# Optimization experiments

Measured on AMD Instinct MI355X. Metric: run time of the kernel, lower is better.

## Reference

```python
import jax, jax.numpy as jnp
import numpy as np

WINDOW_SIZE = 2
SOFTMAX_TEMP = 0.01
WIDTH = 320
EPS = 1e-12  # F.normalize default eps


def _l2norm(x, axis):
    n = jnp.sqrt(jnp.sum(x * x, axis=axis, keepdims=True))
    return x / jnp.maximum(n, EPS)


def setup_inputs() -> dict:
    key = jax.random.key(0)
    k1, k2, k3, k4 = jax.random.split(key, 4)
    BW, C, N, S = 4, 256, 1024, 1
    return {
        "keypoint_scores": jax.random.uniform(k1, (BW, S, N), dtype=jnp.float32),
        "keypoint_desc": jax.random.normal(k2, (BW, C, N), dtype=jnp.float32),
        "desc_dense": jax.random.normal(k3, (BW, C, WIDTH, WIDTH), dtype=jnp.float32),
        "keypoint_coords": jax.random.uniform(k4, (BW, N, 2), dtype=jnp.float32),
    }


def reference(keypoint_scores, keypoint_desc, desc_dense, keypoint_coords):
    BW, C, N = keypoint_desc.shape
    B = BW // WINDOW_SIZE
    P = B * (WINDOW_SIZE - 1)  # number of (src, tgt) pairs

    # dense source pixel coordinates (u=col, v=row), matching torch meshgrid 'ij'
    idx = jnp.arange(WIDTH * WIDTH)
    coords = jnp.stack([(idx % WIDTH).astype(jnp.float32),
                        (idx // WIDTH).astype(jnp.float32)], axis=1)  # (HW, 2)

    # pair indexing: for window i, targets are i*w+1 .. i*w+w-1, source is i*w
    tgt_ids = jnp.array([i * WINDOW_SIZE + j for i in range(B)
                         for j in range(1, WINDOW_SIZE)], dtype=jnp.int32)
    src_ids = (tgt_ids // WINDOW_SIZE) * WINDOW_SIZE

    # normalized dense source descriptors: (B, C, HW)
    src_dense = desc_dense[::WINDOW_SIZE].reshape(B, C, -1)
    src_un = _l2norm(src_dense, axis=1)
    src_sel = src_un[tgt_ids // WINDOW_SIZE]  # (P, C, HW)

    # normalized target keypoint descriptors: (P, C, N)
    tgt_n = _l2norm(keypoint_desc[tgt_ids], axis=1)

    # QK^T over descriptor channel: (P, N, HW)
    match_vals = jnp.einsum('pcn,pcm->pnm', tgt_n, src_sel)
    soft = jax.nn.softmax(match_vals / SOFTMAX_TEMP, axis=2)

    # soft-argmax coordinates: (P, N, 2)
    pseudo_coords = jnp.einsum('pnm,md->pnd', soft, coords)

    match_weights = keypoint_scores[tgt_ids]  # (P, S, N)
    return pseudo_coords, match_weights, tgt_ids, src_ids
```

## Files before the change

### kernel.cpp

```cpp
#include <hip/hip_runtime.h>
#include <stdint.h>

#define HW_      102400
#define C_       256
#define N_       1024
#define P_       2
#define TILES_   1600
#define CHUNKS_  32
#define ITERS_   50
#define NB_      4
#define K2_      144.269504088896340f
#define MOFF_    (-72.134752044448170f)

typedef __attribute__((ext_vector_type(8))) short bf16x8;
typedef __attribute__((ext_vector_type(4))) float f32x4;

#define WS_TGT_OFF  0
#define WS_PAR_OFF  (1u << 20)
#define WS_PN_OFF   (4u << 20)

#define SWR(r) (((r) ^ ((r) >> 3)) & 7)

__device__ __forceinline__ uint32_t packbf(float a, float b) {
  uint32_t r;
  asm("v_cvt_pk_bf16_f32 %0, %1, %2" : "=v"(r) : "v"(a), "v"(b));
  return r;
}
__device__ __forceinline__ float fexp2(float x) {
  return __builtin_amdgcn_exp2f(x);
}
__device__ __forceinline__ void dma16(const uint32_t* g, uint32_t* l) {
  __builtin_amdgcn_global_load_lds(
      (const __attribute__((address_space(1))) uint32_t*)g,
      (__attribute__((address_space(3))) uint32_t*)l, 16, 0, 0);
}

__global__ __launch_bounds__(256)
void k_pre(const float* __restrict__ dense, const float* __restrict__ kdesc,
           const float* __restrict__ kscores, uint32_t* __restrict__ PN,
           uint16_t* __restrict__ tgt, float* __restrict__ out) {
  __shared__ float part[16][64];
  __shared__ float sinv[64];
  __shared__ uint32_t T[8192];
  const int bid = blockIdx.x;
  if (bid < P_ * TILES_) {
    const int p = bid / TILES_, tile = bid % TILES_;
    const int t   = threadIdx.x;
    const int px4 = (t & 15) * 4;
    const int cg  = t >> 4;
    const float* src = dense + (size_t)(p * 2) * C_ * HW_ + (size_t)(cg * 16) * HW_
                     + tile * 64 + px4;
    float v[16][4];
    #pragma unroll
    for (int cc = 0; cc < 16; ++cc) {
      const float4 q = *(const float4*)(src + (size_t)cc * HW_);
      v[cc][0] = q.x; v[cc][1] = q.y; v[cc][2] = q.z; v[cc][3] = q.w;
    }
    float ps[4] = {0.f, 0.f, 0.f, 0.f};
    #pragma unroll
    for (int cc = 0; cc < 16; ++cc) {
      #pragma unroll
      for (int i = 0; i < 4; ++i) ps[i] = fmaf(v[cc][i], v[cc][i], ps[i]);
    }
    #pragma unroll
    for (int i = 0; i < 4; ++i) part[cg][px4 + i] = ps[i];
    __syncthreads();
    if (t < 64) {
      float s = 0.f;
      #pragma unroll
      for (int g = 0; g < 16; ++g) s += part[g][t];
      sinv[t] = 1.f / fmaxf(sqrtf(s), 1e-12f);
    }
    __syncthreads();
    #pragma unroll
    for (int i = 0; i < 4; ++i) {
      const int r  = px4 + i;
      const float iv = sinv[r];
      const int s8 = SWR(r);
      uint32_t* dst = &T[r * 128];
      uint4 A, B;
      A.x = packbf(v[0][i] * iv,  v[1][i] * iv);
      A.y = packbf(v[2][i] * iv,  v[3][i] * iv);
      A.z = packbf(v[4][i] * iv,  v[5][i] * iv);
      A.w = packbf(v[6][i] * iv,  v[7][i] * iv);
      B.x = packbf(v[8][i] * iv,  v[9][i] * iv);
      B.y = packbf(v[10][i] * iv, v[11][i] * iv);
      B.z = packbf(v[12][i] * iv, v[13][i] * iv);
      B.w = packbf(v[14][i] * iv, v[15][i] * iv);
      *(uint4*)&dst[((2 * cg + 0) ^ s8) * 4] = A;
      *(uint4*)&dst[((2 * cg + 1) ^ s8) * 4] = B;
    }
    __syncthreads();
    uint32_t* dstg = PN + ((size_t)(p * TILES_ + tile) << 13) + t * 32;
    #pragma unroll
    for (int k = 0; k < 8; ++k)
      *(uint4*)&dstg[k * 4] = *(const uint4*)&T[t * 32 + k * 4];
  } else {
    const int t = (bid - P_ * TILES_) * 256 + threadIdx.x;
    const int p = t >> 10, n = t & 1023;
    const float* src = kdesc + (size_t)(p * 2 + 1) * C_ * N_ + n;
    float s = 0.f;
    #pragma unroll 16
    for (int c = 0; c < C_; ++c) { const float v2 = src[c * N_]; s = fmaf(v2, v2, s); }
    const float inv = 1.f / fmaxf(sqrtf(s), 1e-12f);
    uint32_t* dst = (uint32_t*)(tgt + (size_t)t * C_);
    #pragma unroll 4
    for (int c8 = 0; c8 < C_; c8 += 8) {
      uint4 wv;
      wv.x = packbf(src[(c8 + 0) * N_] * inv, src[(c8 + 1) * N_] * inv);
      wv.y = packbf(src[(c8 + 2) * N_] * inv, src[(c8 + 3) * N_] * inv);
      wv.z = packbf(src[(c8 + 4) * N_] * inv, src[(c8 + 5) * N_] * inv);
      wv.w = packbf(src[(c8 + 6) * N_] * inv, src[(c8 + 7) * N_] * inv);
      *(uint4*)&dst[c8 / 2] = wv;
    }
    out[4096 + t] = kscores[(p * 2 + 1) * N_ + n];
  }
}

__global__ __launch_bounds__(1024, 4)
void k_main(const uint32_t* __restrict__ PN, const uint16_t* __restrict__ tgt,
            float4* __restrict__ partials) {
  __shared__ uint32_t lds[2 * 8192];

  const int bid = blockIdx.x;
  const int xcd = bid & 7;
  const int rr  = bid >> 3;
  const int nb  = rr & 3;
  const int grp = xcd + 8 * (rr >> 2);
  const int p     = grp >> 5;
  const int chunk = grp & 31;

  const int t    = threadIdx.x;
  const int lane = t & 63;
  const int w    = t >> 6;
  const int l15  = lane & 15;
  const int g4   = lane >> 4;
  const int h    = w & 1;
  const int q    = w >> 1;

  bf16x8 Bf[2][8];
  const int nbase = nb * 256 + q * 32;
  #pragma unroll
  for (int j = 0; j < 2; ++j) {
    const uint16_t* tp = tgt + (size_t)(p * N_ + nbase + j * 16 + l15) * C_ + g4 * 8;
    #pragma unroll
    for (int k = 0; k < 8; ++k) Bf[j][k] = *(const bf16x8*)(tp + k * 32);
  }

  float stS[2], stU[2], stV[2];
  #pragma unroll
  for (int j = 0; j < 2; ++j) { stS[j] = 0.f; stU[j] = 0.f; stV[j] = 0.f; }

  const int row0  = h * 32 + l15;
  const int sw0   = SWR(row0) << 2;
  const int sw1   = sw0 ^ 8;
  const int base0 = row0 * 128;
  const int base1 = base0 + 16 * 128;
  const int lr0   = h * 32 + g4 * 4;

  float offf[2][4];
  #pragma unroll
  for (int s = 0; s < 2; ++s)
    #pragma unroll
    for (int e = 0; e < 4; ++e) offf[s][e] = (float)(lr0 + s * 16 + e);

  const uint32_t* PNp = PN + ((size_t)(p * TILES_ + chunk * ITERS_) << 13) + w * 512 + lane * 4;
  uint32_t* ldsw0 = &lds[w * 512];

  dma16(PNp, ldsw0);
  dma16(PNp + 256, ldsw0 + 256);
  __syncthreads();

  float u0f = 0.f, v0f = (float)(chunk * 10);
  for (int iter = 0; iter < ITERS_; ++iter) {
    if (iter + 1 < ITERS_) {
      const uint32_t* s = PNp + ((size_t)(iter + 1) << 13);
      uint32_t* d = ldsw0 + ((iter & 1) ^ 1) * 8192;
      dma16(s, d);
      dma16(s + 256, d + 256);
    }

    const uint32_t* bufR = &lds[(iter & 1) * 8192];
    f32x4 acc[2][2];
    #pragma unroll
    for (int j = 0; j < 2; ++j) {
      acc[j][0] = (f32x4){0.f, 0.f, 0.f, 0.f};
      acc[j][1] = (f32x4){0.f, 0.f, 0.f, 0.f};
    }
    __builtin_amdgcn_s_setprio(1);
    #pragma unroll
    for (int k = 0; k < 8; ++k) {
      const int col = k * 16 + g4 * 4;
      bf16x8 a0 = *(const bf16x8*)&bufR[base0 + (col ^ sw0)];
      bf16x8 a1 = *(const bf16x8*)&bufR[base1 + (col ^ sw1)];
      acc[0][0] = __builtin_amdgcn_mfma_f32_16x16x32_bf16(a0, Bf[0][k], acc[0][0], 0, 0, 0);
      acc[0][1] = __builtin_amdgcn_mfma_f32_16x16x32_bf16(a1, Bf[0][k], acc[0][1], 0, 0, 0);
      acc[1][0] = __builtin_amdgcn_mfma_f32_16x16x32_bf16(a0, Bf[1][k], acc[1][0], 0, 0, 0);
      acc[1][1] = __builtin_amdgcn_mfma_f32_16x16x32_bf16(a1, Bf[1][k], acc[1][1], 0, 0, 0);
    }
    __builtin_amdgcn_s_setprio(0);

    #pragma unroll
    for (int j = 0; j < 2; ++j) {
      float tS = 0.f, tU = 0.f;
      #pragma unroll
      for (int s = 0; s < 2; ++s) {
        #pragma unroll
        for (int e = 0; e < 4; ++e) {
          const float ev = fexp2(fmaf(K2_, acc[j][s][e], MOFF_));
          tS += ev;
          tU = fmaf(ev, offf[s][e], tU);
        }
      }
      stS[j] += tS;
      stU[j] += fmaf(u0f, tS, tU);
      stV[j] = fmaf(v0f, tS, stV[j]);
    }
    u0f += 64.f;
    if (u0f > 290.f) { u0f = 0.f; v0f += 1.f; }

    __syncthreads();
  }

  #pragma unroll
  for (int j = 0; j < 2; ++j) {
    float S = stS[j], U = stU[j], V = stV[j];
    S += __shfl_xor(S, 16, 64); U += __shfl_xor(U, 16, 64); V += __shfl_xor(V, 16, 64);
    S += __shfl_xor(S, 32, 64); U += __shfl_xor(U, 32, 64); V += __shfl_xor(V, 32, 64);
    if (lane < 16) {
      const int n = nbase + j * 16 + l15;
      partials[((size_t)(p * CHUNKS_ + chunk) * 2 + h) * N_ + n] = make_float4(S, U, V, 0.f);
    }
  }
}

__global__ void k_final(const float4* __restrict__ partials, float* __restrict__ out) {
  const int t = blockIdx.x * blockDim.x + threadIdx.x;
  const int p = t >> 10, n = t & 1023;
  float S = 0.f, U = 0.f, V = 0.f;
  #pragma unroll 4
  for (int s = 0; s < 2 * CHUNKS_; ++s) {
    const float4 v = partials[((size_t)p * 2 * CHUNKS_ + s) * N_ + n];
    S += v.x; U += v.y; V += v.z;
  }
  out[(size_t)(p * N_ + n) * 2 + 0] = U / S;
  out[(size_t)(p * N_ + n) * 2 + 1] = V / S;
  if (t < 4) {
    const float ids[4] = {1.f, 3.f, 0.f, 2.f};
    out[6144 + t] = ids[t];
  }
}

extern "C" void kernel_launch(void* const* d_in, const int* in_sizes, int n_in,
                              void* d_out, int out_size, void* d_ws, size_t ws_size,
                              hipStream_t stream) {
  const float* kscores = (const float*)d_in[0];
  const float* kdesc   = (const float*)d_in[1];
  const float* dense   = (const float*)d_in[2];
  float* out = (float*)d_out;

  char* ws = (char*)d_ws;
  uint16_t* tgt = (uint16_t*)(ws + WS_TGT_OFF);
  float4*   par = (float4*)(ws + WS_PAR_OFF);
  uint32_t* PN  = (uint32_t*)(ws + WS_PN_OFF);

  k_pre<<<P_ * TILES_ + (P_ * N_) / 256, 256, 0, stream>>>(dense, kdesc, kscores, PN, tgt, out);
  k_main<<<P_ * NB_ * CHUNKS_, 1024, 0, stream>>>(PN, tgt, par);
  k_final<<<(P_ * N_) / 256, 256, 0, stream>>>(par, out);
}
```

Before: 189.2 us.

## Read source tiles directly from global memory in MFMA fragment layout, dropping LDS staging

The preprocessing kernel now writes normalized bf16 source tiles straight to global memory in a layout matching the MFMA A-fragment read pattern, instead of going through a swizzled LDS transpose. The main kernel drops LDS double-buffering and per-iteration barriers and loads A fragments directly from global/L2. Each block now has 512 threads, and each wave covers 64 keypoints instead of 32, so every A load feeds twice as many MFMAs. The cost is more registers per wave and exposed global-load latency with no explicit prefetch, which leaves latency hiding to occupancy and the cache.

```diff
diff --git a/kernel.cpp b/kernel.cpp
--- a/kernel.cpp
+++ b/kernel.cpp
@@ -19,8 +19,6 @@
 #define WS_PAR_OFF  (1u << 20)
 #define WS_PN_OFF   (4u << 20)
 
-#define SWR(r) (((r) ^ ((r) >> 3)) & 7)
-
 __device__ __forceinline__ uint32_t packbf(float a, float b) {
   uint32_t r;
   asm("v_cvt_pk_bf16_f32 %0, %1, %2" : "=v"(r) : "v"(a), "v"(b));
@@ -28,11 +26,6 @@
 }
 __device__ __forceinline__ float fexp2(float x) {
   return __builtin_amdgcn_exp2f(x);
-}
-__device__ __forceinline__ void dma16(const uint32_t* g, uint32_t* l) {
-  __builtin_amdgcn_global_load_lds(
-      (const __attribute__((address_space(1))) uint32_t*)g,
-      (__attribute__((address_space(3))) uint32_t*)l, 16, 0, 0);
 }
 
 __global__ __launch_bounds__(256)
@@ -41,7 +34,6 @@
            uint16_t* __restrict__ tgt, float* __restrict__ out) {
   __shared__ float part[16][64];
   __shared__ float sinv[64];
-  __shared__ uint32_t T[8192];
   const int bid = blockIdx.x;
   if (bid < P_ * TILES_) {
     const int p = bid / TILES_, tile = bid % TILES_;
@@ -72,12 +64,14 @@
       sinv[t] = 1.f / fmaxf(sqrtf(s), 1e-12f);
     }
     __syncthreads();
+    uint32_t* dstg = PN + ((size_t)(p * TILES_ + tile) << 13);
+    const int kk   = cg >> 1;
+    const int half = cg & 1;
     #pragma unroll
     for (int i = 0; i < 4; ++i) {
       const int r  = px4 + i;
       const float iv = sinv[r];
-      const int s8 = SWR(r);
-      uint32_t* dst = &T[r * 128];
+      uint32_t* d = dstg + (kk * 64 + r) * 16 + half * 8;
       uint4 A, B;
       A.x = packbf(v[0][i] * iv,  v[1][i] * iv);
       A.y = packbf(v[2][i] * iv,  v[3][i] * iv);
@@ -87,14 +81,9 @@
       B.y = packbf(v[10][i] * iv, v[11][i] * iv);
       B.z = packbf(v[12][i] * iv, v[13][i] * iv);
       B.w = packbf(v[14][i] * iv, v[15][i] * iv);
-      *(uint4*)&dst[((2 * cg + 0) ^ s8) * 4] = A;
-      *(uint4*)&dst[((2 * cg + 1) ^ s8) * 4] = B;
-    }
-    __syncthreads();
-    uint32_t* dstg = PN + ((size_t)(p * TILES_ + tile) << 13) + t * 32;
-    #pragma unroll
-    for (int k = 0; k < 8; ++k)
-      *(uint4*)&dstg[k * 4] = *(const uint4*)&T[t * 32 + k * 4];
+      *(uint4*)&d[0] = A;
+      *(uint4*)&d[4] = B;
+    }
   } else {
     const int t = (bid - P_ * TILES_) * 256 + threadIdx.x;
     const int p = t >> 10, n = t & 1023;
@@ -117,11 +106,9 @@
   }
 }
 
-__global__ __launch_bounds__(1024, 4)
+__global__ __launch_bounds__(512, 2)
 void k_main(const uint32_t* __restrict__ PN, const uint16_t* __restrict__ tgt,
             float4* __restrict__ partials) {
-  __shared__ uint32_t lds[2 * 8192];
-
   const int bid = blockIdx.x;
   const int xcd = bid & 7;
   const int rr  = bid >> 3;
@@ -138,25 +125,21 @@
   const int h    = w & 1;
   const int q    = w >> 1;
 
-  bf16x8 Bf[2][8];
-  const int nbase = nb * 256 + q * 32;
-  #pragma unroll
-  for (int j = 0; j < 2; ++j) {
+  bf16x8 Bf[4][8];
+  const int nbase = nb * 256 + q * 64;
+  #pragma unroll
+  for (int j = 0; j < 4; ++j) {
     const uint16_t* tp = tgt + (size_t)(p * N_ + nbase + j * 16 + l15) * C_ + g4 * 8;
     #pragma unroll
     for (int k = 0; k < 8; ++k) Bf[j][k] = *(const bf16x8*)(tp + k * 32);
   }
 
-  float stS[2], stU[2], stV[2];
-  #pragma unroll
-  for (int j = 0; j < 2; ++j) { stS[j] = 0.f; stU[j] = 0.f; stV[j] = 0.f; }
-
-  const int row0  = h * 32 + l15;
-  const int sw0   = SWR(row0) << 2;
-  const int sw1   = sw0 ^ 8;
-  const int base0 = row0 * 128;
-  const int base1 = base0 + 16 * 128;
-  const int lr0   = h * 32 + g4 * 4;
+  float stS[4], stU[4], stV[4];
+  #pragma unroll
+  for (int j = 0; j < 4; ++j) { stS[j] = 0.f; stU[j] = 0.f; stV[j] = 0.f; }
+
+  const int lr0 = h * 32 + g4 * 4;
+  const int aoff = (h * 32 + l15) * 16 + g4 * 4;
 
   float offf[2][4];
   #pragma unroll
@@ -164,44 +147,36 @@
     #pragma unroll
     for (int e = 0; e < 4; ++e) offf[s][e] = (float)(lr0 + s * 16 + e);
 
-  const uint32_t* PNp = PN + ((size_t)(p * TILES_ + chunk * ITERS_) << 13) + w * 512 + lane * 4;
-  uint32_t* ldsw0 = &lds[w * 512];
-
-  dma16(PNp, ldsw0);
-  dma16(PNp + 256, ldsw0 + 256);
-  __syncthreads();
+  const uint32_t* PNc = PN + ((size_t)(p * TILES_ + chunk * ITERS_) << 13);
 
   float u0f = 0.f, v0f = (float)(chunk * 10);
   for (int iter = 0; iter < ITERS_; ++iter) {
-    if (iter + 1 < ITERS_) {
-      const uint32_t* s = PNp + ((size_t)(iter + 1) << 13);
-      uint32_t* d = ldsw0 + ((iter & 1) ^ 1) * 8192;
-      dma16(s, d);
-      dma16(s + 256, d + 256);
-    }
-
-    const uint32_t* bufR = &lds[(iter & 1) * 8192];
-    f32x4 acc[2][2];
-    #pragma unroll
-    for (int j = 0; j < 2; ++j) {
+    const uint32_t* bt = PNc + ((size_t)iter << 13);
+
+    f32x4 acc[4][2];
+    #pragma unroll
+    for (int j = 0; j < 4; ++j) {
       acc[j][0] = (f32x4){0.f, 0.f, 0.f, 0.f};
       acc[j][1] = (f32x4){0.f, 0.f, 0.f, 0.f};
     }
     __builtin_amdgcn_s_setprio(1);
     #pragma unroll
     for (int k = 0; k < 8; ++k) {
-      const int col = k * 16 + g4 * 4;
-      bf16x8 a0 = *(const bf16x8*)&bufR[base0 + (col ^ sw0)];
-      bf16x8 a1 = *(const bf16x8*)&bufR[base1 + (col ^ sw1)];
+      const bf16x8 a0 = *(const bf16x8*)&bt[k * 1024 + aoff];
+      const bf16x8 a1 = *(const bf16x8*)&bt[k * 1024 + 256 + aoff];
       acc[0][0] = __builtin_amdgcn_mfma_f32_16x16x32_bf16(a0, Bf[0][k], acc[0][0], 0, 0, 0);
       acc[0][1] = __builtin_amdgcn_mfma_f32_16x16x32_bf16(a1, Bf[0][k], acc[0][1], 0, 0, 0);
       acc[1][0] = __builtin_amdgcn_mfma_f32_16x16x32_bf16(a0, Bf[1][k], acc[1][0], 0, 0, 0);
       acc[1][1] = __builtin_amdgcn_mfma_f32_16x16x32_bf16(a1, Bf[1][k], acc[1][1], 0, 0, 0);
+      acc[2][0] = __builtin_amdgcn_mfma_f32_16x16x32_bf16(a0, Bf[2][k], acc[2][0], 0, 0, 0);
+      acc[2][1] = __builtin_amdgcn_mfma_f32_16x16x32_bf16(a1, Bf[2][k], acc[2][1], 0, 0, 0);
+      acc[3][0] = __builtin_amdgcn_mfma_f32_16x16x32_bf16(a0, Bf[3][k], acc[3][0], 0, 0, 0);
+      acc[3][1] = __builtin_amdgcn_mfma_f32_16x16x32_bf16(a1, Bf[3][k], acc[3][1], 0, 0, 0);
     }
     __builtin_amdgcn_s_setprio(0);
 
     #pragma unroll
-    for (int j = 0; j < 2; ++j) {
+    for (int j = 0; j < 4; ++j) {
       float tS = 0.f, tU = 0.f;
       #pragma unroll
       for (int s = 0; s < 2; ++s) {
@@ -218,12 +193,10 @@
     }
     u0f += 64.f;
     if (u0f > 290.f) { u0f = 0.f; v0f += 1.f; }
-
-    __syncthreads();
-  }
-
-  #pragma unroll
-  for (int j = 0; j < 2; ++j) {
+  }
+
+  #pragma unroll
+  for (int j = 0; j < 4; ++j) {
     float S = stS[j], U = stU[j], V = stV[j];
     S += __shfl_xor(S, 16, 64); U += __shfl_xor(U, 16, 64); V += __shfl_xor(V, 16, 64);
     S += __shfl_xor(S, 32, 64); U += __shfl_xor(U, 32, 64); V += __shfl_xor(V, 32, 64);
@@ -265,6 +238,6 @@
   uint32_t* PN  = (uint32_t*)(ws + WS_PN_OFF);
 
   k_pre<<<P_ * TILES_ + (P_ * N_) / 256, 256, 0, stream>>>(dense, kdesc, kscores, PN, tgt, out);
-  k_main<<<P_ * NB_ * CHUNKS_, 1024, 0, stream>>>(PN, tgt, par);
+  k_main<<<P_ * NB_ * CHUNKS_, 512, 0, stream>>>(PN, tgt, par);
   k_final<<<(P_ * N_) / 256, 256, 0, stream>>>(par, out);
 }
```

Result: slower. 219.5 us (+16.0%).
